# Kernel tuning notes

Measured on AMD Instinct MI355X. Metric: run time of the kernel, lower is better.

## Reference

```python
import jax, jax.numpy as jnp
import numpy as np

M_DIM = 1024
H_DIM = 1024
NEG = -1e9


def setup_inputs() -> dict:
    key = jax.random.key(0)
    ks = jax.random.split(key, 9)
    B, S = 4, 2048
    q = jax.random.normal(ks[0], (B, S, M_DIM), dtype=jnp.float32)
    k = jax.random.normal(ks[1], (B, S, M_DIM), dtype=jnp.float32)
    v = jax.random.normal(ks[2], (B, S, M_DIM), dtype=jnp.float32)
    attention_mask = jnp.ones((B, S), dtype=jnp.int32)
    sc = 1.0 / np.sqrt(M_DIM)
    Wq_w = jax.random.normal(ks[3], (H_DIM, M_DIM), dtype=jnp.float32) * sc
    Wq_b = jnp.zeros((H_DIM,), dtype=jnp.float32)
    Wk_w = jax.random.normal(ks[4], (H_DIM, M_DIM), dtype=jnp.float32) * sc
    Wk_b = jnp.zeros((H_DIM,), dtype=jnp.float32)
    Wv_w = jax.random.normal(ks[5], (H_DIM, M_DIM), dtype=jnp.float32) * sc
    Wv_b = jnp.zeros((H_DIM,), dtype=jnp.float32)
    return {"q": q, "k": k, "v": v, "attention_mask": attention_mask,
            "Wq_w": Wq_w, "Wq_b": Wq_b, "Wk_w": Wk_w, "Wk_b": Wk_b,
            "Wv_w": Wv_w, "Wv_b": Wv_b}


def reference(q, k, v, attention_mask, Wq_w, Wq_b, Wk_w, Wk_b, Wv_w, Wv_b):
    # Linear projections (torch Linear: x @ W.T + b)
    qh = jnp.einsum('bsm,hm->bsh', q, Wq_w) + Wq_b
    kh = jnp.einsum('bsm,hm->bsh', k, Wk_w) + Wk_b
    vh = jnp.einsum('bsm,hm->bsh', v, Wv_w) + Wv_b
    # Scaled dot-product scores: [B, Sq, Sk]
    scores = jnp.einsum('bqh,bkh->bqk', qh, kh) / jnp.sqrt(jnp.float32(H_DIM))
    # Padding mask: attention_mask [B, Sk] -> [B, 1, Sk]
    pad = attention_mask.astype(bool)[:, None, :]
    scores = jnp.where(pad, scores, NEG)
    # Causal mask (apply_mask=True)
    Sq, Sk = scores.shape[1], scores.shape[2]
    causal = jnp.tril(jnp.ones((Sq, Sk), dtype=bool))
    scores = jnp.where(causal[None, :, :], scores, NEG)
    attn = jax.nn.softmax(scores, axis=-1)
    out = jnp.einsum('bqk,bkh->bqh', attn, vh)
    # dropout is identity in eval mode
    return out
```

## Files before the change

### kernel.cpp

```cpp
#include <hip/hip_runtime.h>
#include <stdint.h>


typedef __attribute__((ext_vector_type(8))) short s8v;
typedef __attribute__((ext_vector_type(4))) float f4v;

__device__ __forceinline__ unsigned short f2bf(float f) {
    union { float f; unsigned u; } v; v.f = f;
    unsigned u = v.u;
    u = u + 0x7fffu + ((u >> 16) & 1u);
    return (unsigned short)(u >> 16);
}

__device__ __forceinline__ void gld_lds16(const void* gptr, void* lptr) {
    __builtin_amdgcn_global_load_lds(
        (const __attribute__((address_space(1))) unsigned int*)(uintptr_t)gptr,
        (__attribute__((address_space(3))) unsigned int*)(unsigned int)(uintptr_t)lptr,
        16, 0, 0);
}

__global__ __launch_bounds__(256) void convert_all(
    const float* __restrict__ q, const float* __restrict__ k, const float* __restrict__ v,
    const float* __restrict__ wq, const float* __restrict__ wk, const float* __restrict__ wv,
    unsigned short* __restrict__ qb, unsigned short* __restrict__ kb, unsigned short* __restrict__ vb,
    unsigned short* __restrict__ wqb, unsigned short* __restrict__ wkb, unsigned short* __restrict__ wvb,
    float* __restrict__ l)
{
    int b = blockIdx.x;
    if (b >= 13824) {
        int li = (b - 13824) * 2048 + threadIdx.x * 8;
        float4 z = {0.f, 0.f, 0.f, 0.f};
        *(float4*)(l + li) = z;
        *(float4*)(l + li + 4) = z;
        return;
    }
    const float* src; unsigned short* dst; int blk;
    if (b < 4096)       { src = q;  dst = qb;  blk = b; }
    else if (b < 8192)  { src = k;  dst = kb;  blk = b - 4096; }
    else if (b < 12288) { src = v;  dst = vb;  blk = b - 8192; }
    else if (b < 12800) { src = wq; dst = wqb; blk = b - 12288; }
    else if (b < 13312) { src = wk; dst = wkb; blk = b - 12800; }
    else                { src = wv; dst = wvb; blk = b - 13312; }
    size_t idx = (size_t)blk * 2048 + (size_t)threadIdx.x * 8;
    float4 f0 = *(const float4*)(src + idx);
    float4 f1 = *(const float4*)(src + idx + 4);
    s8v o;
    o[0] = (short)f2bf(f0.x); o[1] = (short)f2bf(f0.y);
    o[2] = (short)f2bf(f0.z); o[3] = (short)f2bf(f0.w);
    o[4] = (short)f2bf(f1.x); o[5] = (short)f2bf(f1.y);
    o[6] = (short)f2bf(f1.z); o[7] = (short)f2bf(f1.w);
    *(s8v*)(dst + idx) = o;
}

__device__ __forceinline__ void gemm_tiles(
    const unsigned short* __restrict__ A, int lda,
    const unsigned short* __restrict__ Bt, int ldb,
    int m0, int n0, int kTiles,
    unsigned short* As, unsigned short* Bs,
    f4v acc[4][4])
{
    const int t    = threadIdx.x;
    const int lane = t & 63;
    const int wave = t >> 6;
    const int wm   = (wave >> 1) * 64;
    const int wn   = (wave & 1) * 64;
    const int l15  = lane & 15;
    const int quad = lane >> 4;

    const int c0 = t, c1 = t + 256;
    unsigned short* As0 = As + (c0 & ~63) * 8;
    unsigned short* As1 = As + (c1 & ~63) * 8;
    unsigned short* Bs0 = Bs + (c0 & ~63) * 8;
    unsigned short* Bs1 = Bs + (c1 & ~63) * 8;
    const unsigned short* Ag0 = A  + (size_t)(m0 + (c0 >> 2)) * lda + (c0 & 3) * 8;
    const unsigned short* Ag1 = A  + (size_t)(m0 + (c1 >> 2)) * lda + (c1 & 3) * 8;
    const unsigned short* Bg0 = Bt + (size_t)(n0 + (c0 >> 2)) * ldb + (c0 & 3) * 8;
    const unsigned short* Bg1 = Bt + (size_t)(n0 + (c1 >> 2)) * ldb + (c1 & 3) * 8;

    const unsigned short* a_base = As + quad * 8;
    const unsigned short* b_base = Bs + quad * 8;

    gld_lds16(Ag0, As0);
    gld_lds16(Ag1, As1);
    gld_lds16(Bg0, Bs0);
    gld_lds16(Bg1, Bs1);

    for (int kt = 0; kt < kTiles; ++kt) {
        __syncthreads();
        Ag0 += 32; Ag1 += 32; Bg0 += 32; Bg1 += 32;
        if (kt + 1 < kTiles) {
            const int nb = ((kt + 1) & 1) * 4096;
            gld_lds16(Ag0, As0 + nb);
            gld_lds16(Ag1, As1 + nb);
            gld_lds16(Bg0, Bs0 + nb);
            gld_lds16(Bg1, Bs1 + nb);
        }
        const int cb = (kt & 1) * 4096;
        s8v af[4], bf[4];
        #pragma unroll
        for (int i = 0; i < 4; ++i)
            af[i] = *(const s8v*)(a_base + cb + (wm + i * 16 + l15) * 32);
        #pragma unroll
        for (int j = 0; j < 4; ++j)
            bf[j] = *(const s8v*)(b_base + cb + (wn + j * 16 + l15) * 32);
        #pragma unroll
        for (int i = 0; i < 4; ++i)
            #pragma unroll
            for (int j = 0; j < 4; ++j)
                acc[i][j] = __builtin_amdgcn_mfma_f32_16x16x32_bf16(af[i], bf[j], acc[i][j], 0, 0, 0);
    }
}

#define ACC_INIT  f4v acc[4][4]; { f4v z = {0.f,0.f,0.f,0.f}; \
    _Pragma("unroll") for (int i = 0; i < 4; ++i) \
    _Pragma("unroll") for (int j = 0; j < 4; ++j) acc[i][j] = z; }

#define LANE_VARS \
    const int lane = threadIdx.x & 63; const int wave = threadIdx.x >> 6; \
    const int wm = (wave >> 1) * 64;  const int wn = (wave & 1) * 64; \
    const int l15 = lane & 15;        const int quad = lane >> 4;

__global__ __launch_bounds__(512, 2) void proj_qk(
    const unsigned short* __restrict__ qb, const unsigned short* __restrict__ wqb,
    const float* __restrict__ bq, unsigned short* __restrict__ QH,
    const unsigned short* __restrict__ kb, const unsigned short* __restrict__ wkb,
    const float* __restrict__ bk, unsigned short* __restrict__ KH)
{
    const int w_ = blockIdx.x;
    const int yz = w_ & 7;
    const int ny = yz & 3;
    const int z  = yz >> 2;
    const int mx = w_ >> 3;
    const unsigned short* X; const unsigned short* W; const float* bias; unsigned short* Y;
    if (z == 0) { X = qb; W = wqb; bias = bq; Y = QH; }
    else        { X = kb; W = wkb; bias = bk; Y = KH; }

    __shared__ __align__(16) unsigned short As[2 * 256 * 64];
    __shared__ __align__(16) unsigned short Bs[2 * 256 * 64];

    const int t    = threadIdx.x;
    const int lane = t & 63;
    const int w    = t >> 6;
    const int wm   = (w >> 2) * 128;
    const int wn   = (w & 3) * 64;
    const int l15  = lane & 15;
    const int quad = lane >> 4;
    const int m0   = mx * 256;
    const int n0   = ny * 256;
    enum { KT = 16 };

    const int r0 = t >> 3;
    const int sw = (t & 7) ^ (r0 & 7);
    const unsigned short* gA = X + (size_t)(m0 + r0) * 1024 + sw * 8;
    const unsigned short* gB = W + (size_t)(n0 + r0) * 1024 + sw * 8;
    unsigned short* lA = As + (t & ~63) * 8;
    unsigned short* lB = Bs + (t & ~63) * 8;

#define PSTAGE_A(b, h, kt) { \
    gld_lds16(gA + (size_t)(h) * 131072 + (kt) * 64,         lA + (b) * 16384 + (h) * 8192); \
    gld_lds16(gA + (size_t)(h) * 131072 + 65536 + (kt) * 64, lA + (b) * 16384 + (h) * 8192 + 4096); }
#define PSTAGE_B(b, h, kt) { \
    gld_lds16(gB + (size_t)(h) * 131072 + (kt) * 64,         lB + (b) * 16384 + (h) * 8192); \
    gld_lds16(gB + (size_t)(h) * 131072 + 65536 + (kt) * 64, lB + (b) * 16384 + (h) * 8192 + 4096); }

    const int aoff = (wm + l15) * 64;
    const int boff = (wn + l15) * 64;
    const int seg0 = ((quad    ) ^ (l15 & 7)) * 8;
    const int seg1 = ((quad | 4) ^ (l15 & 7)) * 8;

    f4v acc[8][4];
    { f4v zz = {0.f, 0.f, 0.f, 0.f};
      #pragma unroll
      for (int i = 0; i < 8; ++i)
        #pragma unroll
        for (int j = 0; j < 4; ++j) acc[i][j] = zz; }
    s8v a[8], b0[4], b1[4];

    PSTAGE_A(0, 0, 0); PSTAGE_A(0, 1, 0); PSTAGE_B(0, 0, 0); PSTAGE_B(0, 1, 0);
    PSTAGE_B(1, 0, 1); PSTAGE_A(1, 0, 1);
    asm volatile("s_waitcnt vmcnt(4)" ::: "memory");
    __builtin_amdgcn_s_barrier();

    for (int kt = 0; kt < KT; ++kt) {
        const int p  = kt & 1;
        const int np = p ^ 1;
        const unsigned short* Ar = As + p * 16384 + aoff;
        const unsigned short* Br = Bs + p * 16384 + boff;

        #pragma unroll
        for (int i = 0; i < 4; ++i) {
            a[i * 2]     = *(const s8v*)(Ar + i * 1024 + seg0);
            a[i * 2 + 1] = *(const s8v*)(Ar + i * 1024 + seg1);
        }
        #pragma unroll
        for (int j = 0; j < 2; ++j) {
            b0[j * 2]     = *(const s8v*)(Br + j * 1024 + seg0);
            b0[j * 2 + 1] = *(const s8v*)(Br + j * 1024 + seg1);
        }
        #pragma unroll
        for (int j = 0; j < 2; ++j) {
            b1[j * 2]     = *(const s8v*)(Br + 2048 + j * 1024 + seg0);
            b1[j * 2 + 1] = *(const s8v*)(Br + 2048 + j * 1024 + seg1);
        }
        if (kt + 1 < KT) PSTAGE_A(np, 1, kt + 1);
        __builtin_amdgcn_s_setprio(1);
        #pragma unroll
        for (int i = 0; i < 4; ++i)
            #pragma unroll
            for (int j = 0; j < 2; ++j) {
                acc[i][j] = __builtin_amdgcn_mfma_f32_16x16x32_bf16(a[i*2],   b0[j*2],   acc[i][j], 0, 0, 0);
                acc[i][j] = __builtin_amdgcn_mfma_f32_16x16x32_bf16(a[i*2+1], b0[j*2+1], acc[i][j], 0, 0, 0);
            }
        __builtin_amdgcn_s_setprio(0);
        if (kt + 1 < KT) PSTAGE_B(np, 1, kt + 1);
        __builtin_amdgcn_s_setprio(1);
        #pragma unroll
        for (int i = 0; i < 4; ++i)
            #pragma unroll
            for (int j = 0; j < 2; ++j) {
                acc[i][2+j] = __builtin_amdgcn_mfma_f32_16x16x32_bf16(a[i*2],   b1[j*2],   acc[i][2+j], 0, 0, 0);
                acc[i][2+j] = __builtin_amdgcn_mfma_f32_16x16x32_bf16(a[i*2+1], b1[j*2+1], acc[i][2+j], 0, 0, 0);
            }
        __builtin_amdgcn_s_setprio(0);
        #pragma unroll
        for (int i = 0; i < 4; ++i) {
            a[i * 2]     = *(const s8v*)(Ar + 4096 + i * 1024 + seg0);
            a[i * 2 + 1] = *(const s8v*)(Ar + 4096 + i * 1024 + seg1);
        }
        __builtin_amdgcn_s_barrier();
        if (kt + 2 < KT) PSTAGE_B(p, 0, kt + 2);
        __builtin_amdgcn_s_setprio(1);
        #pragma unroll
        for (int i = 0; i < 4; ++i)
            #pragma unroll
            for (int j = 0; j < 2; ++j) {
                acc[4+i][2+j] = __builtin_amdgcn_mfma_f32_16x16x32_bf16(a[i*2],   b1[j*2],   acc[4+i][2+j], 0, 0, 0);
                acc[4+i][2+j] = __builtin_amdgcn_mfma_f32_16x16x32_bf16(a[i*2+1], b1[j*2+1], acc[4+i][2+j], 0, 0, 0);
            }
        __builtin_amdgcn_s_setprio(0);
        __builtin_amdgcn_s_barrier();
        if (kt + 2 < KT) PSTAGE_A(p, 0, kt + 2);
        __builtin_amdgcn_s_setprio(1);
        #pragma unroll
        for (int i = 0; i < 4; ++i)
            #pragma unroll
            for (int j = 0; j < 2; ++j) {
                acc[4+i][j] = __builtin_amdgcn_mfma_f32_16x16x32_bf16(a[i*2],   b0[j*2],   acc[4+i][j], 0, 0, 0);
                acc[4+i][j] = __builtin_amdgcn_mfma_f32_16x16x32_bf16(a[i*2+1], b0[j*2+1], acc[4+i][j], 0, 0, 0);
            }
        __builtin_amdgcn_s_setprio(0);
        if (kt + 2 < KT) { asm volatile("s_waitcnt vmcnt(4)" ::: "memory"); }
        else             { asm volatile("s_waitcnt vmcnt(0)" ::: "memory"); }
        __builtin_amdgcn_s_barrier();
    }
#undef PSTAGE_A
#undef PSTAGE_B

    #pragma unroll
    for (int ig = 0; ig < 8; ++ig) {
        int row = m0 + wm + ig * 16 + quad * 4;
        #pragma unroll
        for (int jg = 0; jg < 4; ++jg) {
            int col = n0 + wn + jg * 16 + l15;
            float bvv = bias[col];
            #pragma unroll
            for (int r = 0; r < 4; ++r)
                Y[(size_t)(row + r) * 1024 + col] = f2bf(acc[ig][jg][r] + bvv);
        }
    }
}

__global__ __launch_bounds__(256) void proj_v(
    const unsigned short* __restrict__ vb, const unsigned short* __restrict__ wvb,
    const float* __restrict__ bv, unsigned short* __restrict__ VHT)
{
    __shared__ __align__(16) unsigned short As[2 * 128 * 32];
    __shared__ __align__(16) unsigned short Bs[2 * 128 * 32];
    const int w_ = blockIdx.x;
    const int m0 = (w_ >> 3) * 128;
    const int n0 = (w_ & 7) * 128;
    ACC_INIT;
    gemm_tiles(vb, 1024, wvb, 1024, m0, n0, 32, As, Bs, acc);
    LANE_VARS;
    #pragma unroll
    for (int i = 0; i < 4; ++i) {
        int row = m0 + wm + i * 16 + quad * 4;
        int bb = row >> 11;
        int s  = row & 2047;
        #pragma unroll
        for (int j = 0; j < 4; ++j) {
            int col = n0 + wn + j * 16 + l15;
            float bvv = bv[col];
            ushort4 o = make_ushort4(f2bf(acc[i][j][0] + bvv), f2bf(acc[i][j][1] + bvv),
                                     f2bf(acc[i][j][2] + bvv), f2bf(acc[i][j][3] + bvv));
            *(ushort4*)(VHT + (size_t)bb * (1024 * 2048) + (size_t)col * 2048 + s) = o;
        }
    }
}

__global__ __launch_bounds__(256) void score_kernel(
    const unsigned short* __restrict__ QH, const unsigned short* __restrict__ KH,
    const int* __restrict__ mask, unsigned short* __restrict__ P, float* __restrict__ lsum)
{
    const int b = blockIdx.y;
    const int bx = blockIdx.x;
    int tq = (bx & 7) * 17 + (bx >> 3);
    int qt = 0;
    while ((qt + 1) * (qt + 2) / 2 <= tq) ++qt;
    const int kt = tq - qt * (qt + 1) / 2;

    __shared__ __align__(16) unsigned short As[2 * 128 * 32];
    __shared__ __align__(16) unsigned short Bs[2 * 128 * 32];
    const unsigned short* A  = QH + (size_t)b * 2048 * 1024;
    const unsigned short* Bt = KH + (size_t)b * 2048 * 1024;
    unsigned short* Pb = P + (size_t)b * 2048 * 2048;
    float* lb = lsum + b * 2048;
    const int* mb = mask + b * 2048;
    const int m0 = qt * 128, n0 = kt * 128;
    ACC_INIT;
    gemm_tiles(A, 1024, Bt, 1024, m0, n0, 32, As, Bs, acc);
    LANE_VARS;
    float rs[4][4];
    #pragma unroll
    for (int i = 0; i < 4; ++i)
        #pragma unroll
        for (int r = 0; r < 4; ++r) rs[i][r] = 0.f;
    #pragma unroll
    for (int i = 0; i < 4; ++i) {
        int qbase = m0 + wm + i * 16 + quad * 4;
        #pragma unroll
        for (int j = 0; j < 4; ++j) {
            int kg = n0 + wn + j * 16 + l15;
            int mv = mb[kg];
            #pragma unroll
            for (int r = 0; r < 4; ++r) {
                float s = acc[i][j][r] * 0.03125f;
                float p = (mv && (kg <= qbase + r)) ? __expf(s) : 0.f;
                Pb[(size_t)(qbase + r) * 2048 + kg] = f2bf(p);
                rs[i][r] += p;
            }
        }
    }
    #pragma unroll
    for (int i = 0; i < 4; ++i)
        #pragma unroll
        for (int r = 0; r < 4; ++r) {
            float v_ = rs[i][r];
            v_ += __shfl_xor(v_, 1);
            v_ += __shfl_xor(v_, 2);
            v_ += __shfl_xor(v_, 4);
            v_ += __shfl_xor(v_, 8);
            if (l15 == 0)
                atomicAdd(&lb[m0 + wm + i * 16 + quad * 4 + r], v_);
        }
}

__constant__ int pv_qt[24] = {15,15, 7,14,14,13,13, 6,12,12,11,11, 5,10,10, 9, 9, 4, 8, 8, 3, 2, 1, 0};
__constant__ int pv_ks[24] = { 0,32, 0, 0,30, 0,28, 0, 0,26, 0,24, 0, 0,22, 0,20, 0, 0,18, 0, 0, 0, 0};
__constant__ int pv_kc[24] = {32,32,32,30,30,28,28,28,26,26,24,24,24,22,22,20,20,20,18,18,16,12, 8, 4};

__global__ __launch_bounds__(256) void pv_kernel(
    const unsigned short* __restrict__ P, const unsigned short* __restrict__ VHT,
    const float* __restrict__ lsum, float* __restrict__ Out, float* __restrict__ Part)
{
    const int w_  = blockIdx.x;
    const int nt  = w_ & 7;
    const int idx = w_ >> 3;
    const int b   = idx / 24;
    const int y   = idx % 24;
    const int qt = pv_qt[y], kstart = pv_ks[y], kcount = pv_kc[y];

    __shared__ __align__(16) unsigned short As[2 * 128 * 32];
    __shared__ __align__(16) unsigned short Bs[2 * 128 * 32];
    const unsigned short* A  = P   + (size_t)b * 2048 * 2048 + (size_t)kstart * 32;
    const unsigned short* Bt = VHT + (size_t)b * 1024 * 2048 + (size_t)kstart * 32;
    const float* lb = lsum + b * 2048;
    const int m0 = qt * 128, n0 = nt * 128;
    ACC_INIT;
    gemm_tiles(A, 2048, Bt, 2048, m0, n0, kcount, As, Bs, acc);
    LANE_VARS;
    float* dst; int rowoff;
    if (kstart == 0) { dst = Out  + (size_t)b * 2048 * 1024; rowoff = 0; }
    else             { dst = Part + (size_t)b * 1024 * 1024; rowoff = -1024; }
    #pragma unroll
    for (int i = 0; i < 4; ++i) {
        int q0 = m0 + wm + i * 16 + quad * 4;
        float inv[4];
        #pragma unroll
        for (int r = 0; r < 4; ++r) inv[r] = 1.0f / lb[q0 + r];
        #pragma unroll
        for (int j = 0; j < 4; ++j) {
            int h = n0 + wn + j * 16 + l15;
            #pragma unroll
            for (int r = 0; r < 4; ++r)
                dst[(size_t)(q0 + r + rowoff) * 1024 + h] = acc[i][j][r] * inv[r];
        }
    }
}

__global__ __launch_bounds__(256) void add_partial(
    float4* __restrict__ Out4, const float4* __restrict__ Part4)
{
    int i = blockIdx.x * 256 + threadIdx.x;
    int b = i >> 18;
    int rem = i & 262143;
    int oi = b * 524288 + 262144 + rem;
    float4 o = Out4[oi], p = Part4[i];
    o.x += p.x; o.y += p.y; o.z += p.z; o.w += p.w;
    Out4[oi] = o;
}

extern "C" void kernel_launch(void* const* d_in, const int* in_sizes, int n_in,
                              void* d_out, int out_size, void* d_ws, size_t ws_size,
                              hipStream_t stream)
{
    const float* q    = (const float*)d_in[0];
    const float* k    = (const float*)d_in[1];
    const float* v    = (const float*)d_in[2];
    const int*   mask = (const int*)d_in[3];
    const float* Wq   = (const float*)d_in[4];
    const float* bq   = (const float*)d_in[5];
    const float* Wk   = (const float*)d_in[6];
    const float* bk   = (const float*)d_in[7];
    const float* Wv   = (const float*)d_in[8];
    const float* bv   = (const float*)d_in[9];
    float* out = (float*)d_out;

    char* ws = (char*)d_ws;
    size_t off = 0;
    auto take = [&](size_t bytes) { char* p = ws + off; off += (bytes + 255) & ~(size_t)255; return p; };
    unsigned short* qb  = (unsigned short*)take(8192ull * 1024 * 2);
    unsigned short* kb  = (unsigned short*)take(8192ull * 1024 * 2);
    unsigned short* vb  = (unsigned short*)take(8192ull * 1024 * 2);
    unsigned short* wqb = (unsigned short*)take(1024ull * 1024 * 2);
    unsigned short* wkb = (unsigned short*)take(1024ull * 1024 * 2);
    unsigned short* wvb = (unsigned short*)take(1024ull * 1024 * 2);
    unsigned short* QH  = (unsigned short*)take(8192ull * 1024 * 2);
    unsigned short* KH  = (unsigned short*)take(8192ull * 1024 * 2);
    unsigned short* VHT = (unsigned short*)take(8192ull * 1024 * 2);
    unsigned short* P   = (unsigned short*)take(4ull * 2048 * 2048 * 2);
    float*          l   = (float*)take(4ull * 2048 * 4);
    float*          Part = (float*)qb;

    convert_all<<<13828, 256, 0, stream>>>(q, k, v, Wq, Wk, Wv,
                                           qb, kb, vb, wqb, wkb, wvb, l);
    proj_qk<<<256, 512, 0, stream>>>(qb, wqb, bq, QH,
                                     kb, wkb, bk, KH);
    proj_v<<<512, 256, 0, stream>>>(vb, wvb, bv, VHT);
    score_kernel<<<dim3(136, 4), 256, 0, stream>>>(QH, KH, mask, P, l);
    pv_kernel<<<768, 256, 0, stream>>>(P, VHT, l, out, Part);
    add_partial<<<4096, 256, 0, stream>>>((float4*)out, (const float4*)Part);
}
```

Before: 300.8 us.

## Drop split-K partials in PV kernel and use causal tile ordering

Replaces the table-driven PV work decomposition, which split long causal rows into two K halves and used a separate add_partial kernel, with one block per (batch, q-tile, n-tile). Blocks are ordered longest-first, then shortest, to balance load. This removes the extra partial-sum writes and reads and one kernel launch. The cost is 512 blocks instead of 768, so the longest tiles run their full K range on one block and tail imbalance may grow on a 256-CU device.

```diff
diff --git a/kernel.cpp b/kernel.cpp
--- a/kernel.cpp
+++ b/kernel.cpp
@@ -355,33 +355,30 @@
         }
 }
 
-__constant__ int pv_qt[24] = {15,15, 7,14,14,13,13, 6,12,12,11,11, 5,10,10, 9, 9, 4, 8, 8, 3, 2, 1, 0};
-__constant__ int pv_ks[24] = { 0,32, 0, 0,30, 0,28, 0, 0,26, 0,24, 0, 0,22, 0,20, 0, 0,18, 0, 0, 0, 0};
-__constant__ int pv_kc[24] = {32,32,32,30,30,28,28,28,26,26,24,24,24,22,22,20,20,20,18,18,16,12, 8, 4};
-
 __global__ __launch_bounds__(256) void pv_kernel(
     const unsigned short* __restrict__ P, const unsigned short* __restrict__ VHT,
-    const float* __restrict__ lsum, float* __restrict__ Out, float* __restrict__ Part)
-{
-    const int w_  = blockIdx.x;
-    const int nt  = w_ & 7;
-    const int idx = w_ >> 3;
-    const int b   = idx / 24;
-    const int y   = idx % 24;
-    const int qt = pv_qt[y], kstart = pv_ks[y], kcount = pv_kc[y];
+    const float* __restrict__ lsum, float* __restrict__ Out)
+{
+    const int w_   = blockIdx.x;
+    const int nt   = w_ & 7;
+    const int u    = w_ >> 3;
+    const int half = u >> 5;
+    const int i_   = u & 31;
+    const int b    = i_ >> 3;
+    const int j_   = i_ & 7;
+    const int qt   = half ? j_ : 15 - j_;
+    const int kcount = 4 * (qt + 1);
 
     __shared__ __align__(16) unsigned short As[2 * 128 * 32];
     __shared__ __align__(16) unsigned short Bs[2 * 128 * 32];
-    const unsigned short* A  = P   + (size_t)b * 2048 * 2048 + (size_t)kstart * 32;
-    const unsigned short* Bt = VHT + (size_t)b * 1024 * 2048 + (size_t)kstart * 32;
+    const unsigned short* A  = P   + (size_t)b * 2048 * 2048;
+    const unsigned short* Bt = VHT + (size_t)b * 1024 * 2048;
     const float* lb = lsum + b * 2048;
     const int m0 = qt * 128, n0 = nt * 128;
     ACC_INIT;
     gemm_tiles(A, 2048, Bt, 2048, m0, n0, kcount, As, Bs, acc);
     LANE_VARS;
-    float* dst; int rowoff;
-    if (kstart == 0) { dst = Out  + (size_t)b * 2048 * 1024; rowoff = 0; }
-    else             { dst = Part + (size_t)b * 1024 * 1024; rowoff = -1024; }
+    float* dst = Out + (size_t)b * 2048 * 1024;
     #pragma unroll
     for (int i = 0; i < 4; ++i) {
         int q0 = m0 + wm + i * 16 + quad * 4;
@@ -393,21 +390,9 @@
             int h = n0 + wn + j * 16 + l15;
             #pragma unroll
             for (int r = 0; r < 4; ++r)
-                dst[(size_t)(q0 + r + rowoff) * 1024 + h] = acc[i][j][r] * inv[r];
-        }
-    }
-}
-
-__global__ __launch_bounds__(256) void add_partial(
-    float4* __restrict__ Out4, const float4* __restrict__ Part4)
-{
-    int i = blockIdx.x * 256 + threadIdx.x;
-    int b = i >> 18;
-    int rem = i & 262143;
-    int oi = b * 524288 + 262144 + rem;
-    float4 o = Out4[oi], p = Part4[i];
-    o.x += p.x; o.y += p.y; o.z += p.z; o.w += p.w;
-    Out4[oi] = o;
+                dst[(size_t)(q0 + r) * 1024 + h] = acc[i][j][r] * inv[r];
+        }
+    }
 }
 
 extern "C" void kernel_launch(void* const* d_in, const int* in_sizes, int n_in,
@@ -440,7 +425,6 @@
     unsigned short* VHT = (unsigned short*)take(8192ull * 1024 * 2);
     unsigned short* P   = (unsigned short*)take(4ull * 2048 * 2048 * 2);
     float*          l   = (float*)take(4ull * 2048 * 4);
-    float*          Part = (float*)qb;
 
     convert_all<<<13828, 256, 0, stream>>>(q, k, v, Wq, Wk, Wv,
                                            qb, kb, vb, wqb, wkb, wvb, l);
@@ -448,6 +432,5 @@
                                      kb, wkb, bk, KH);
     proj_v<<<512, 256, 0, stream>>>(vb, wvb, bv, VHT);
     score_kernel<<<dim3(136, 4), 256, 0, stream>>>(QH, KH, mask, P, l);
-    pv_kernel<<<768, 256, 0, stream>>>(P, VHT, l, out, Part);
-    add_partial<<<4096, 256, 0, stream>>>((float4*)out, (const float4*)Part);
-}
+    pv_kernel<<<512, 256, 0, stream>>>(P, VHT, l, out);
+}
```

New measurement: 289.5 us. 1.04x faster.
